# Performance work log

Measured on AMD Instinct MI355X. Metric: run time of the kernel, lower is better.

The kernel has to match this reference:

```python
import jax, jax.numpy as jnp
import numpy as np

CH = 512      # input channels
V = 320       # codewords per group
G = 2         # groups
CV_DIM = 256  # codevector_dim (wav2vec2 default)
D = CV_DIM // G
TAU = 2.0     # gumbel temperature


def setup_inputs() -> dict:
    key = jax.random.key(0)
    k1, k2, k3, k4 = jax.random.split(key, 4)
    B, T = 32, 1024
    x = jax.random.normal(k1, (B, T, CH), jnp.float32)
    W_proj = jax.random.normal(k2, (CH, G * V), jnp.float32) / np.sqrt(CH)
    b_proj = jnp.zeros((G * V,), jnp.float32)
    codevectors = jax.random.normal(k3, (G, V, D), jnp.float32) * 0.02
    # uniform noise, transformed to Gumbel inside reference
    u_noise = jax.random.uniform(k4, (B, T, G, V), jnp.float32,
                                 minval=1e-6, maxval=1.0 - 1e-6)
    return {"x": x, "W_proj": W_proj, "b_proj": b_proj,
            "codevectors": codevectors, "u_noise": u_noise}


def reference(x, W_proj, b_proj, codevectors, u_noise):
    B, T, _ = x.shape
    # projection to per-group logits: [B,T,G,V]
    logits = (x @ W_proj + b_proj).reshape(B, T, G, V)
    # gumbel-softmax (hard, straight-through)
    g = -jnp.log(-jnp.log(u_noise))
    soft = jax.nn.softmax((logits + g) / TAU, axis=-1)
    hard = jax.nn.one_hot(jnp.argmax(soft, axis=-1), V, dtype=soft.dtype)
    st = hard + soft - jax.lax.stop_gradient(soft)
    # combine selected codewords per group, concat groups -> [B,T,CV_DIM]
    out = jnp.einsum('btgv,gvd->btgd', st, codevectors).reshape(B, T, G * D)
    return out
```

## Files before the change

kernel.cpp:

```cpp
#include <hip/hip_runtime.h>
#include <cmath>

namespace {

typedef _Float16 half8 __attribute__((ext_vector_type(8)));
typedef float f32x4 __attribute__((ext_vector_type(4)));

constexpr int M_TOTAL = 32 * 1024;
constexpr int K_CH    = 512;
constexpr int NV      = 640;
constexpr int D_CV    = 128;
constexpr int NSLOT   = 10;

constexpr int BM = 128, BN = 128, BK = 32;
constexpr int NTILE  = NV / BN;
constexpr int NPANEL = M_TOTAL / BM;
constexpr int NBLK   = NTILE * NPANEL;
constexpr int KT     = K_CH / BK;

constexpr float LO_SCALE = 4096.0f;
constexpr float LO_INV   = 1.0f / 4096.0f;

__device__ __forceinline__ void gld16(const void* g, void* l) {
  __builtin_amdgcn_global_load_lds(
      (__attribute__((address_space(1))) void*)g,
      (__attribute__((address_space(3))) void*)l, 16, 0, 0);
}

__global__ __launch_bounds__(256)
void prep_w(const float* __restrict__ W, _Float16* __restrict__ Wth,
            _Float16* __restrict__ Wtl)
{
  __shared__ float tile[32][33];
  const int bk = blockIdx.x & 15;
  const int bn = blockIdx.x >> 4;
  const int k0 = bk * 32, n0 = bn * 32;
  const int t = threadIdx.x;
  const int nn = t & 31, kk = t >> 5;
  #pragma unroll
  for (int p = 0; p < 4; ++p)
    tile[kk + p * 8][nn] = W[(size_t)(k0 + kk + p * 8) * NV + n0 + nn];
  __syncthreads();
  const int kx = t & 31, nx = t >> 5;
  #pragma unroll
  for (int p = 0; p < 4; ++p) {
    const float v = tile[kx][nx + p * 8];
    const _Float16 h = (_Float16)v;
    const _Float16 l = (_Float16)((v - (float)h) * LO_SCALE);
    const size_t o = (size_t)(n0 + nx + p * 8) * K_CH + k0 + kx;
    Wth[o] = h;
    Wtl[o] = l;
  }
}

__global__ __launch_bounds__(256, 2)
void gvq_mfma3(const float* __restrict__ x,
               const _Float16* __restrict__ Wth, const _Float16* __restrict__ Wtl,
               const float* __restrict__ bias, const float* __restrict__ u,
               float* __restrict__ pval, int* __restrict__ pidx)
{
  __shared__ __align__(16) float    As[2][BM * BK];
  __shared__ __align__(16) _Float16 Bhs[2][BN * BK];
  __shared__ __align__(16) _Float16 Bls[2][BN * BK];

  const int chunk = NBLK / 8;
  const int nid   = (blockIdx.x % 8) * chunk + blockIdx.x / 8;
  const int panel = nid / NTILE, ntile = nid % NTILE;
  const int m0 = panel * BM, n0 = ntile * BN;

  const int t    = threadIdx.x;
  const int wv   = t >> 6, lane = t & 63;
  const int wr   = wv >> 1, wc = wv & 1;
  const int li   = lane & 15, q = lane >> 4;

  const int arow = t >> 3;
  const int akc  = (t & 7) ^ ((t >> 3) & 7);
  const int brow = t >> 2;
  const int bkc  = (t & 3) ^ ((t >> 3) & 3);

  const float*    pxa = x   + (size_t)(m0 + arow) * K_CH + akc * 4;
  const _Float16* pbh = Wth + (size_t)(n0 + brow) * K_CH + bkc * 8;
  const _Float16* pbl = Wtl + (size_t)(n0 + brow) * K_CH + bkc * 8;

  f32x4 acc1[4][4];
  f32x4 acc2[4][4];
  #pragma unroll
  for (int i = 0; i < 4; ++i)
    #pragma unroll
    for (int j = 0; j < 4; ++j) {
      acc1[i][j] = (f32x4){0.f, 0.f, 0.f, 0.f};
      acc2[i][j] = (f32x4){0.f, 0.f, 0.f, 0.f};
    }

  auto stage = [&](int kt, int b) {
    const int ko = kt * BK;
    #pragma unroll
    for (int i = 0; i < 4; ++i)
      gld16(pxa + (size_t)i * 32 * K_CH + ko,
            &As[b][(i * 256 + wv * 64) * 4]);
    #pragma unroll
    for (int i = 0; i < 2; ++i) {
      gld16(pbh + (size_t)i * 64 * K_CH + ko,
            &Bhs[b][(i * 256 + wv * 64) * 8]);
      gld16(pbl + (size_t)i * 64 * K_CH + ko,
            &Bls[b][(i * 256 + wv * 64) * 8]);
    }
  };

  stage(0, 0);
  __syncthreads();
  int buf = 0;
  for (int kt = 0; kt < KT; ++kt) {
    if (kt + 1 < KT) stage(kt + 1, buf ^ 1);

    half8 bhv[4], blv[4];
    #pragma unroll
    for (int fn = 0; fn < 4; ++fn) {
      const int rb  = wc * 64 + fn * 16 + li;
      const int off = rb * 32 + ((q ^ ((rb >> 1) & 3)) << 3);
      bhv[fn] = *reinterpret_cast<const half8*>(&Bhs[buf][off]);
      blv[fn] = *reinterpret_cast<const half8*>(&Bls[buf][off]);
    }

    #pragma unroll
    for (int fm = 0; fm < 4; ++fm) {
      const int ra = wr * 64 + fm * 16 + li;
      const int sa = ra & 7;
      const f32x4 f0 = *reinterpret_cast<const f32x4*>(
          &As[buf][ra * 32 + (((q * 2 + 0) ^ sa) << 2)]);
      const f32x4 f1 = *reinterpret_cast<const f32x4*>(
          &As[buf][ra * 32 + (((q * 2 + 1) ^ sa) << 2)]);
      half8 ah, al;
      #pragma unroll
      for (int e = 0; e < 4; ++e) {
        float v = f0[e];
        _Float16 h = (_Float16)v;
        ah[e] = h; al[e] = (_Float16)((v - (float)h) * LO_SCALE);
        v = f1[e];
        h = (_Float16)v;
        ah[4 + e] = h; al[4 + e] = (_Float16)((v - (float)h) * LO_SCALE);
      }
      #pragma unroll
      for (int fn = 0; fn < 4; ++fn) {
        acc1[fm][fn] = __builtin_amdgcn_mfma_f32_16x16x32_f16(
            ah, bhv[fn], acc1[fm][fn], 0, 0, 0);
        acc2[fm][fn] = __builtin_amdgcn_mfma_f32_16x16x32_f16(
            ah, blv[fn], acc2[fm][fn], 0, 0, 0);
        acc2[fm][fn] = __builtin_amdgcn_mfma_f32_16x16x32_f16(
            al, bhv[fn], acc2[fm][fn], 0, 0, 0);
      }
    }
    __syncthreads();
    buf ^= 1;
  }

  const int colbase = n0 + wc * 64 + li;
  float bb[4];
  #pragma unroll
  for (int fn = 0; fn < 4; ++fn) bb[fn] = bias[colbase + fn * 16];

  const int slot = ntile * 2 + wc;
  #pragma unroll
  for (int fm = 0; fm < 4; ++fm) {
    #pragma unroll
    for (int r = 0; r < 4; ++r) {
      const int m = m0 + wr * 64 + fm * 16 + q * 4 + r;
      float bv = -INFINITY;
      int   bi = 0x7fffffff;
      #pragma unroll
      for (int fn = 0; fn < 4; ++fn) {
        const float uu  = u[(size_t)m * NV + colbase + fn * 16];
        const float g   = -__logf(-__logf(uu));
        const float val = acc1[fm][fn][r] + acc2[fm][fn][r] * LO_INV
                          + bb[fn] + g;
        const int   n   = colbase + fn * 16;
        if (val > bv) { bv = val; bi = n; }
      }
      #pragma unroll
      for (int s = 1; s <= 8; s <<= 1) {
        const float ov = __shfl_xor(bv, s);
        const int   oi = __shfl_xor(bi, s);
        if (ov > bv || (ov == bv && oi < bi)) { bv = ov; bi = oi; }
      }
      if (li == 0) {
        pval[(size_t)m * NSLOT + slot] = bv;
        pidx[(size_t)m * NSLOT + slot] = bi;
      }
    }
  }
}

__global__ __launch_bounds__(256)
void gvq_gather(const float* __restrict__ pval,
                const int*   __restrict__ pidx,
                const float* __restrict__ cv,
                float* __restrict__ out)
{
  const int tid  = threadIdx.x;
  const int w    = tid >> 6;
  const int lane = tid & 63;
  const int m    = blockIdx.x * 4 + w;
  const int g    = lane >> 5;

  const float* pv = &pval[(size_t)m * NSLOT + g * 5];
  const int*   pi = &pidx[(size_t)m * NSLOT + g * 5];
  float bv = pv[0];
  int   bi = pi[0];
  #pragma unroll
  for (int s = 1; s < 5; ++s) {
    const float v = pv[s];
    const int   i = pi[s];
    if (v > bv || (v == bv && i < bi)) { bv = v; bi = i; }
  }
  const float4 src = *reinterpret_cast<const float4*>(
      &cv[(size_t)bi * D_CV + (lane & 31) * 4]);
  *reinterpret_cast<float4*>(&out[(size_t)m * 256 + lane * 4]) = src;
}

}

extern "C" void kernel_launch(void* const* d_in, const int* in_sizes, int n_in,
                              void* d_out, int out_size, void* d_ws, size_t ws_size,
                              hipStream_t stream)
{
  const float* x    = (const float*)d_in[0];
  const float* W    = (const float*)d_in[1];
  const float* bias = (const float*)d_in[2];
  const float* cv   = (const float*)d_in[3];
  const float* u    = (const float*)d_in[4];
  float* out = (float*)d_out;

  _Float16* Wth  = (_Float16*)d_ws;
  _Float16* Wtl  = Wth + (size_t)NV * K_CH;
  float*    pval = (float*)(Wtl + (size_t)NV * K_CH);
  int*      pidx = (int*)(pval + (size_t)M_TOTAL * NSLOT);

  hipLaunchKernelGGL(prep_w, dim3(320), dim3(256), 0, stream, W, Wth, Wtl);
  hipLaunchKernelGGL(gvq_mfma3, dim3(NBLK), dim3(256), 0, stream,
                     x, Wth, Wtl, bias, u, pval, pidx);
  hipLaunchKernelGGL(gvq_gather, dim3(M_TOTAL / 4), dim3(256), 0, stream,
                     pval, pidx, cv, out);
}
```

Measured before the change: 136.9 us.

## Pre-split x into fp16 hi/lo and deepen GEMM prefetch pipeline

```diff
diff --git a/kernel.cpp b/kernel.cpp
--- a/kernel.cpp
+++ b/kernel.cpp
@@ -4,6 +4,7 @@
 namespace {
 
 typedef _Float16 half8 __attribute__((ext_vector_type(8)));
+typedef _Float16 half4v __attribute__((ext_vector_type(4)));
 typedef float f32x4 __attribute__((ext_vector_type(4)));
 
 constexpr int M_TOTAL = 32 * 1024;
@@ -53,15 +54,34 @@
   }
 }
 
+__global__ __launch_bounds__(256)
+void prep_x(const float* __restrict__ x, _Float16* __restrict__ Xh,
+            _Float16* __restrict__ Xl)
+{
+  const size_t i = ((size_t)blockIdx.x * 256 + threadIdx.x) * 2;
+  #pragma unroll
+  for (int j = 0; j < 2; ++j) {
+    const float4 v = reinterpret_cast<const float4*>(x)[i + j];
+    const float* pv = &v.x;
+    half4v h, l;
+    #pragma unroll
+    for (int e = 0; e < 4; ++e) {
+      const _Float16 hh = (_Float16)pv[e];
+      h[e] = hh;
+      l[e] = (_Float16)((pv[e] - (float)hh) * LO_SCALE);
+    }
+    reinterpret_cast<half4v*>(Xh)[i + j] = h;
+    reinterpret_cast<half4v*>(Xl)[i + j] = l;
+  }
+}
+
 __global__ __launch_bounds__(256, 2)
-void gvq_mfma3(const float* __restrict__ x,
+void gvq_mfma4(const _Float16* __restrict__ Xh, const _Float16* __restrict__ Xl,
                const _Float16* __restrict__ Wth, const _Float16* __restrict__ Wtl,
                const float* __restrict__ bias, const float* __restrict__ u,
                float* __restrict__ pval, int* __restrict__ pidx)
 {
-  __shared__ __align__(16) float    As[2][BM * BK];
-  __shared__ __align__(16) _Float16 Bhs[2][BN * BK];
-  __shared__ __align__(16) _Float16 Bls[2][BN * BK];
+  __shared__ __align__(16) _Float16 lds[2][16384];
 
   const int chunk = NBLK / 8;
   const int nid   = (blockIdx.x % 8) * chunk + blockIdx.x / 8;
@@ -73,14 +93,16 @@
   const int wr   = wv >> 1, wc = wv & 1;
   const int li   = lane & 15, q = lane >> 4;
 
-  const int arow = t >> 3;
-  const int akc  = (t & 7) ^ ((t >> 3) & 7);
-  const int brow = t >> 2;
-  const int bkc  = (t & 3) ^ ((t >> 3) & 3);
-
-  const float*    pxa = x   + (size_t)(m0 + arow) * K_CH + akc * 4;
-  const _Float16* pbh = Wth + (size_t)(n0 + brow) * K_CH + bkc * 8;
-  const _Float16* pbl = Wtl + (size_t)(n0 + brow) * K_CH + bkc * 8;
+  const int r0 = t >> 2;
+  const int gc = (t & 3) ^ ((t >> 3) & 3);
+  const _Float16* pxh0 = Xh  + (size_t)(m0 + r0) * K_CH + gc * 8;
+  const _Float16* pxh1 = Xh  + (size_t)(m0 + 64 + r0) * K_CH + gc * 8;
+  const _Float16* pxl0 = Xl  + (size_t)(m0 + r0) * K_CH + gc * 8;
+  const _Float16* pxl1 = Xl  + (size_t)(m0 + 64 + r0) * K_CH + gc * 8;
+  const _Float16* pbh0 = Wth + (size_t)(n0 + r0) * K_CH + gc * 8;
+  const _Float16* pbh1 = Wth + (size_t)(n0 + 64 + r0) * K_CH + gc * 8;
+  const _Float16* pbl0 = Wtl + (size_t)(n0 + r0) * K_CH + gc * 8;
+  const _Float16* pbl1 = Wtl + (size_t)(n0 + 64 + r0) * K_CH + gc * 8;
 
   f32x4 acc1[4][4];
   f32x4 acc2[4][4];
@@ -94,64 +116,54 @@
 
   auto stage = [&](int kt, int b) {
     const int ko = kt * BK;
-    #pragma unroll
-    for (int i = 0; i < 4; ++i)
-      gld16(pxa + (size_t)i * 32 * K_CH + ko,
-            &As[b][(i * 256 + wv * 64) * 4]);
-    #pragma unroll
-    for (int i = 0; i < 2; ++i) {
-      gld16(pbh + (size_t)i * 64 * K_CH + ko,
-            &Bhs[b][(i * 256 + wv * 64) * 8]);
-      gld16(pbl + (size_t)i * 64 * K_CH + ko,
-            &Bls[b][(i * 256 + wv * 64) * 8]);
-    }
+    _Float16* L = &lds[b][0];
+    gld16(pxh0 + ko, L + 0     + wv * 512);
+    gld16(pxh1 + ko, L + 2048  + wv * 512);
+    gld16(pxl0 + ko, L + 4096  + wv * 512);
+    gld16(pxl1 + ko, L + 6144  + wv * 512);
+    gld16(pbh0 + ko, L + 8192  + wv * 512);
+    gld16(pbh1 + ko, L + 10240 + wv * 512);
+    gld16(pbl0 + ko, L + 12288 + wv * 512);
+    gld16(pbl1 + ko, L + 14336 + wv * 512);
   };
 
+  const int soff = ((q ^ ((li >> 1) & 3)) << 3);
+  const int arow = (wr * 64 + li) * 32;
+  const int brow = (wc * 64 + li) * 32;
+
   stage(0, 0);
-  __syncthreads();
-  int buf = 0;
+  stage(1, 1);
+  #pragma unroll
   for (int kt = 0; kt < KT; ++kt) {
-    if (kt + 1 < KT) stage(kt + 1, buf ^ 1);
-
-    half8 bhv[4], blv[4];
-    #pragma unroll
-    for (int fn = 0; fn < 4; ++fn) {
-      const int rb  = wc * 64 + fn * 16 + li;
-      const int off = rb * 32 + ((q ^ ((rb >> 1) & 3)) << 3);
-      bhv[fn] = *reinterpret_cast<const half8*>(&Bhs[buf][off]);
-      blv[fn] = *reinterpret_cast<const half8*>(&Bls[buf][off]);
-    }
-
-    #pragma unroll
-    for (int fm = 0; fm < 4; ++fm) {
-      const int ra = wr * 64 + fm * 16 + li;
-      const int sa = ra & 7;
-      const f32x4 f0 = *reinterpret_cast<const f32x4*>(
-          &As[buf][ra * 32 + (((q * 2 + 0) ^ sa) << 2)]);
-      const f32x4 f1 = *reinterpret_cast<const f32x4*>(
-          &As[buf][ra * 32 + (((q * 2 + 1) ^ sa) << 2)]);
-      half8 ah, al;
-      #pragma unroll
-      for (int e = 0; e < 4; ++e) {
-        float v = f0[e];
-        _Float16 h = (_Float16)v;
-        ah[e] = h; al[e] = (_Float16)((v - (float)h) * LO_SCALE);
-        v = f1[e];
-        h = (_Float16)v;
-        ah[4 + e] = h; al[4 + e] = (_Float16)((v - (float)h) * LO_SCALE);
-      }
+    const int cur = kt & 1;
+    if (kt < KT - 1) asm volatile("s_waitcnt vmcnt(8)" ::: "memory");
+    else             asm volatile("s_waitcnt vmcnt(0)" ::: "memory");
+    __builtin_amdgcn_s_barrier();
+    __builtin_amdgcn_sched_barrier(0);
+
+    const _Float16* L = &lds[cur][0];
+    half8 ah[4], al[4], bh[4], bl[4];
+    #pragma unroll
+    for (int f = 0; f < 4; ++f) {
+      ah[f] = *reinterpret_cast<const half8*>(L + arow + f * 512 + soff);
+      al[f] = *reinterpret_cast<const half8*>(L + 4096  + arow + f * 512 + soff);
+      bh[f] = *reinterpret_cast<const half8*>(L + 8192  + brow + f * 512 + soff);
+      bl[f] = *reinterpret_cast<const half8*>(L + 12288 + brow + f * 512 + soff);
+    }
+    #pragma unroll
+    for (int fm = 0; fm < 4; ++fm)
       #pragma unroll
       for (int fn = 0; fn < 4; ++fn) {
         acc1[fm][fn] = __builtin_amdgcn_mfma_f32_16x16x32_f16(
-            ah, bhv[fn], acc1[fm][fn], 0, 0, 0);
+            ah[fm], bh[fn], acc1[fm][fn], 0, 0, 0);
         acc2[fm][fn] = __builtin_amdgcn_mfma_f32_16x16x32_f16(
-            ah, blv[fn], acc2[fm][fn], 0, 0, 0);
+            ah[fm], bl[fn], acc2[fm][fn], 0, 0, 0);
         acc2[fm][fn] = __builtin_amdgcn_mfma_f32_16x16x32_f16(
-            al, bhv[fn], acc2[fm][fn], 0, 0, 0);
-      }
-    }
-    __syncthreads();
-    buf ^= 1;
+            al[fm], bh[fn], acc2[fm][fn], 0, 0, 0);
+      }
+    __builtin_amdgcn_sched_barrier(0);
+    __builtin_amdgcn_s_barrier();
+    if (kt + 2 < KT) stage(kt + 2, cur);
   }
 
   const int colbase = n0 + wc * 64 + li;
@@ -234,10 +246,13 @@
   _Float16* Wtl  = Wth + (size_t)NV * K_CH;
   float*    pval = (float*)(Wtl + (size_t)NV * K_CH);
   int*      pidx = (int*)(pval + (size_t)M_TOTAL * NSLOT);
+  _Float16* Xh   = (_Float16*)(pidx + (size_t)M_TOTAL * NSLOT);
+  _Float16* Xl   = Xh + (size_t)M_TOTAL * K_CH;
 
   hipLaunchKernelGGL(prep_w, dim3(320), dim3(256), 0, stream, W, Wth, Wtl);
-  hipLaunchKernelGGL(gvq_mfma3, dim3(NBLK), dim3(256), 0, stream,
-                     x, Wth, Wtl, bias, u, pval, pidx);
+  hipLaunchKernelGGL(prep_x, dim3(8192), dim3(256), 0, stream, x, Xh, Xl);
+  hipLaunchKernelGGL(gvq_mfma4, dim3(NBLK), dim3(256), 0, stream,
+                     Xh, Xl, Wth, Wtl, bias, u, pval, pidx);
   hipLaunchKernelGGL(gvq_gather, dim3(M_TOTAL / 4), dim3(256), 0, stream,
                      pval, pidx, cv, out);
 }
```

Measured after the change: 133.5 us. -2.5%, faster.

## Prefetch two k-tiles ahead with explicit vmcnt waits and register-staged LDS reads

Applied to the files above, without the earlier changes.

```diff
diff --git a/kernel.cpp b/kernel.cpp
--- a/kernel.cpp
+++ b/kernel.cpp
@@ -54,14 +54,12 @@
 }
 
 __global__ __launch_bounds__(256, 2)
-void gvq_mfma3(const float* __restrict__ x,
+void gvq_mfma9(const float* __restrict__ x,
                const _Float16* __restrict__ Wth, const _Float16* __restrict__ Wtl,
                const float* __restrict__ bias, const float* __restrict__ u,
                float* __restrict__ pval, int* __restrict__ pidx)
 {
-  __shared__ __align__(16) float    As[2][BM * BK];
-  __shared__ __align__(16) _Float16 Bhs[2][BN * BK];
-  __shared__ __align__(16) _Float16 Bls[2][BN * BK];
+  __shared__ __align__(16) char lds[2][32768];
 
   const int chunk = NBLK / 8;
   const int nid   = (blockIdx.x % 8) * chunk + blockIdx.x / 8;
@@ -73,14 +71,11 @@
   const int wr   = wv >> 1, wc = wv & 1;
   const int li   = lane & 15, q = lane >> 4;
 
-  const int arow = t >> 3;
-  const int akc  = (t & 7) ^ ((t >> 3) & 7);
-  const int brow = t >> 2;
-  const int bkc  = (t & 3) ^ ((t >> 3) & 3);
-
-  const float*    pxa = x   + (size_t)(m0 + arow) * K_CH + akc * 4;
-  const _Float16* pbh = Wth + (size_t)(n0 + brow) * K_CH + bkc * 8;
-  const _Float16* pbl = Wtl + (size_t)(n0 + brow) * K_CH + bkc * 8;
+  const int gca = (t & 7) ^ ((t >> 3) & 7);
+  const float* pxa = x + (size_t)(m0 + (t >> 3)) * K_CH + gca * 4;
+  const int gcb = (t & 3) ^ ((t >> 3) & 3);
+  const _Float16* pbh = Wth + (size_t)(n0 + (t >> 2)) * K_CH + gcb * 8;
+  const _Float16* pbl = Wtl + (size_t)(n0 + (t >> 2)) * K_CH + gcb * 8;
 
   f32x4 acc1[4][4];
   f32x4 acc2[4][4];
@@ -94,64 +89,72 @@
 
   auto stage = [&](int kt, int b) {
     const int ko = kt * BK;
+    char* L = lds[b];
     #pragma unroll
     for (int i = 0; i < 4; ++i)
-      gld16(pxa + (size_t)i * 32 * K_CH + ko,
-            &As[b][(i * 256 + wv * 64) * 4]);
+      gld16(pxa + (size_t)i * 32 * K_CH + ko, L + i * 4096 + wv * 1024);
     #pragma unroll
     for (int i = 0; i < 2; ++i) {
-      gld16(pbh + (size_t)i * 64 * K_CH + ko,
-            &Bhs[b][(i * 256 + wv * 64) * 8]);
-      gld16(pbl + (size_t)i * 64 * K_CH + ko,
-            &Bls[b][(i * 256 + wv * 64) * 8]);
+      gld16(pbh + (size_t)i * 64 * K_CH + ko, L + 16384 + i * 4096 + wv * 1024);
+      gld16(pbl + (size_t)i * 64 * K_CH + ko, L + 24576 + i * 4096 + wv * 1024);
     }
   };
 
+  const int abase = (wr * 64 + li) * 128;
+  const int s0 = (((q * 2 + 0) ^ (li & 7)) << 4);
+  const int s1 = (((q * 2 + 1) ^ (li & 7)) << 4);
+  const int bboff = (wc * 64 + li) * 64 + ((q ^ ((li >> 1) & 3)) << 4);
+
   stage(0, 0);
-  __syncthreads();
-  int buf = 0;
+  stage(1, 1);
+  #pragma unroll
   for (int kt = 0; kt < KT; ++kt) {
-    if (kt + 1 < KT) stage(kt + 1, buf ^ 1);
-
-    half8 bhv[4], blv[4];
+    const int cur = kt & 1;
+    if (kt < KT - 1) asm volatile("s_waitcnt vmcnt(8)" ::: "memory");
+    else             asm volatile("s_waitcnt vmcnt(0)" ::: "memory");
+    __builtin_amdgcn_s_barrier();
+
+    const char* L = lds[cur];
+    half8 bh[4], bl[4];
+    f32x4 af0[4], af1[4];
     #pragma unroll
     for (int fn = 0; fn < 4; ++fn) {
-      const int rb  = wc * 64 + fn * 16 + li;
-      const int off = rb * 32 + ((q ^ ((rb >> 1) & 3)) << 3);
-      bhv[fn] = *reinterpret_cast<const half8*>(&Bhs[buf][off]);
-      blv[fn] = *reinterpret_cast<const half8*>(&Bls[buf][off]);
-    }
-
+      bh[fn] = *reinterpret_cast<const half8*>(L + 16384 + fn * 1024 + bboff);
+      bl[fn] = *reinterpret_cast<const half8*>(L + 24576 + fn * 1024 + bboff);
+    }
     #pragma unroll
     for (int fm = 0; fm < 4; ++fm) {
-      const int ra = wr * 64 + fm * 16 + li;
-      const int sa = ra & 7;
-      const f32x4 f0 = *reinterpret_cast<const f32x4*>(
-          &As[buf][ra * 32 + (((q * 2 + 0) ^ sa) << 2)]);
-      const f32x4 f1 = *reinterpret_cast<const f32x4*>(
-          &As[buf][ra * 32 + (((q * 2 + 1) ^ sa) << 2)]);
+      af0[fm] = *reinterpret_cast<const f32x4*>(L + abase + fm * 2048 + s0);
+      af1[fm] = *reinterpret_cast<const f32x4*>(L + abase + fm * 2048 + s1);
+    }
+    asm volatile("s_waitcnt lgkmcnt(0)" ::: "memory");
+    __builtin_amdgcn_sched_barrier(0);
+    __builtin_amdgcn_s_barrier();
+
+    if (kt + 2 < KT) stage(kt + 2, cur);
+
+    __builtin_amdgcn_s_setprio(1);
+    #pragma unroll
+    for (int fm = 0; fm < 4; ++fm) {
       half8 ah, al;
       #pragma unroll
       for (int e = 0; e < 4; ++e) {
-        float v = f0[e];
-        _Float16 h = (_Float16)v;
-        ah[e] = h; al[e] = (_Float16)((v - (float)h) * LO_SCALE);
-        v = f1[e];
-        h = (_Float16)v;
-        ah[4 + e] = h; al[4 + e] = (_Float16)((v - (float)h) * LO_SCALE);
+        const float v0 = af0[fm][e], v1 = af1[fm][e];
+        const _Float16 h0 = (_Float16)v0, h1 = (_Float16)v1;
+        ah[e]     = h0; al[e]     = (_Float16)((v0 - (float)h0) * LO_SCALE);
+        ah[4 + e] = h1; al[4 + e] = (_Float16)((v1 - (float)h1) * LO_SCALE);
       }
       #pragma unroll
       for (int fn = 0; fn < 4; ++fn) {
         acc1[fm][fn] = __builtin_amdgcn_mfma_f32_16x16x32_f16(
-            ah, bhv[fn], acc1[fm][fn], 0, 0, 0);
+            ah, bh[fn], acc1[fm][fn], 0, 0, 0);
         acc2[fm][fn] = __builtin_amdgcn_mfma_f32_16x16x32_f16(
-            ah, blv[fn], acc2[fm][fn], 0, 0, 0);
+            ah, bl[fn], acc2[fm][fn], 0, 0, 0);
         acc2[fm][fn] = __builtin_amdgcn_mfma_f32_16x16x32_f16(
-            al, bhv[fn], acc2[fm][fn], 0, 0, 0);
-      }
-    }
-    __syncthreads();
-    buf ^= 1;
+            al, bh[fn], acc2[fm][fn], 0, 0, 0);
+      }
+    }
+    __builtin_amdgcn_s_setprio(0);
   }
 
   const int colbase = n0 + wc * 64 + li;
@@ -236,7 +239,7 @@
   int*      pidx = (int*)(pval + (size_t)M_TOTAL * NSLOT);
 
   hipLaunchKernelGGL(prep_w, dim3(320), dim3(256), 0, stream, W, Wth, Wtl);
-  hipLaunchKernelGGL(gvq_mfma3, dim3(NBLK), dim3(256), 0, stream,
+  hipLaunchKernelGGL(gvq_mfma9, dim3(NBLK), dim3(256), 0, stream,
                      x, Wth, Wtl, bias, u, pval, pidx);
   hipLaunchKernelGGL(gvq_gather, dim3(M_TOTAL / 4), dim3(256), 0, stream,
                      pval, pidx, cv, out);
```

Result: faster. 124.3 us (-9.2%).
